# Kernel optimization log

Hardware: AMD Instinct MI355X
Metric: run time of the kernel (lower is better)

Reference implementation:

```python
import jax, jax.numpy as jnp
import numpy as np

K = 8192          # num_codes
D = 256           # code_dim
COMMIT_BETA = 0.25


def setup_inputs() -> dict:
    key = jax.random.key(0)
    k1, k2 = jax.random.split(key)
    z_e = jax.random.normal(k1, (16, 2048, D), dtype=jnp.float32)
    # nn.init.normal_(weight, mean=0, std=1/sqrt(D))
    codebook = jax.random.normal(k2, (K, D), dtype=jnp.float32) * (1.0 / D ** 0.5)
    return {"z_e": z_e, "codebook": codebook}


def reference(z_e, codebook):
    lead_shape = z_e.shape[:-1]
    flat = z_e.reshape(-1, D)                                   # (N, D)
    dist = (
        jnp.sum(flat * flat, axis=-1, keepdims=True)
        - 2.0 * flat @ codebook.T
        + jnp.sum(codebook * codebook, axis=-1)
    )
    idx = jnp.argmin(dist, axis=-1).reshape(lead_shape)          # (...,) int
    z_q = codebook[idx]                                          # (..., D)
    codebook_loss = jnp.mean((z_q - jax.lax.stop_gradient(z_e)) ** 2)
    commit_loss = jnp.mean((z_e - jax.lax.stop_gradient(z_q)) ** 2)
    loss = codebook_loss + COMMIT_BETA * commit_loss
    # straight-through estimator
    z_q_ste = z_e + jax.lax.stop_gradient(z_q - z_e)
    return z_q_ste, idx, loss
```

## Files before the change

kernel.cpp:

```cpp
#include <hip/hip_runtime.h>


#define N_TOK   32768
#define KC      8192
#define DD      256
#define D4      64
#define CSPL    2
#define MT      128
#define EPS1    0.025f
#define EPS2    1e-3f
#define FLAG_CAP 8192
#define CAP2     4096
#define ASTR    40

typedef __bf16    bf16x8 __attribute__((ext_vector_type(8)));
typedef _Float16  f16x8  __attribute__((ext_vector_type(8)));
typedef _Float16  f16x4  __attribute__((ext_vector_type(4)));
typedef float     f32x4  __attribute__((ext_vector_type(4)));

#define GLL(gp, lp) __builtin_amdgcn_global_load_lds(                                   \
    (const __attribute__((address_space(1))) void*)(unsigned long long)(uintptr_t)(gp), \
    (__attribute__((address_space(3))) void*)(unsigned)(uintptr_t)(lp), 16, 0, 0)

#define PK(a, b, HO, LO) do {                                   \
    unsigned ua = __float_as_uint(a), ub = __float_as_uint(b);  \
    unsigned ham = ua & 0xFFFF0000u, hbm = ub & 0xFFFF0000u;    \
    float la = (a) - __uint_as_float(ham);                      \
    float lb = (b) - __uint_as_float(hbm);                      \
    HO = (ua >> 16) | hbm;                                      \
    LO = (__float_as_uint(la) >> 16) | (__float_as_uint(lb) & 0xFFFF0000u); \
} while (0)

__global__ __launch_bounds__(256)
void k_cnorm(const float* __restrict__ cb, float* __restrict__ cnorm,
             double* __restrict__ accum, int* __restrict__ flagc,
             int* __restrict__ flagc2, _Float16* __restrict__ cbf16) {
    if (blockIdx.x == 0 && threadIdx.x == 0) { *accum = 0.0; *flagc = 0; *flagc2 = 0; }
    const int gid  = blockIdx.x * 256 + threadIdx.x;
    const int code = gid >> 6;
    const int lane = threadIdx.x & 63;
    if (code < KC) {
        float4 v = ((const float4*)cb)[code * D4 + lane];
        if (cbf16) {
            f16x4 h;
            h[0] = (_Float16)v.x; h[1] = (_Float16)v.y;
            h[2] = (_Float16)v.z; h[3] = (_Float16)v.w;
            *(f16x4*)(cbf16 + (size_t)code * DD + lane * 4) = h;
        }
        float s = v.x*v.x + v.y*v.y + v.z*v.z + v.w*v.w;
        #pragma unroll
        for (int off = 32; off > 0; off >>= 1) s += __shfl_down(s, off);
        if (lane == 0) cnorm[code] = s;
    }
}

__global__ __launch_bounds__(256)
void k_convert_ze(const float* __restrict__ src, _Float16* __restrict__ dst, int n8) {
    int t = blockIdx.x * 256 + threadIdx.x;
    if (t >= n8) return;
    const float4* s = (const float4*)src;
    float4 v0 = s[2 * t], v1 = s[2 * t + 1];
    f16x8 h;
    h[0] = (_Float16)v0.x; h[1] = (_Float16)v0.y; h[2] = (_Float16)v0.z; h[3] = (_Float16)v0.w;
    h[4] = (_Float16)v1.x; h[5] = (_Float16)v1.y; h[6] = (_Float16)v1.z; h[7] = (_Float16)v1.w;
    ((f16x8*)dst)[t] = h;
}

__global__ __launch_bounds__(256)
void k_argmin_f16(const _Float16* __restrict__ zef, const _Float16* __restrict__ cbf,
                  const float* __restrict__ cnorm, float4* __restrict__ partial) {
    __shared__ __align__(16) char smem[65536];

    const int tid  = threadIdx.x;
    const int lane = tid & 63;
    const int wid  = tid >> 6;
    const int cl   = lane & 15;
    const int kq   = lane >> 4;
    const int m0   = blockIdx.x * MT;
    const int split = blockIdx.y;
    const int c0b  = split * (KC / CSPL);
    const int wrow0 = wid * 32;

    {
        const int lr = lane >> 5;
        const int lc = lane & 31;
        #pragma unroll
        for (int j = 0; j < 16; ++j) {
            int I = wid * 16 + j;
            int r = 2 * I + lr;
            int c = lc ^ (r & 31);
            GLL((const char*)zef + (size_t)(m0 + r) * 512 + c * 16, smem + I * 1024);
        }
    }
    __syncthreads();
    f16x8 afr[2][8];
    #pragma unroll
    for (int mt = 0; mt < 2; ++mt)
        #pragma unroll
        for (int ks = 0; ks < 8; ++ks) {
            int row = wrow0 + mt * 16 + cl;
            int c   = ks * 4 + kq;
            afr[mt][ks] = *(const f16x8*)(smem + row * 512 + (((c ^ (row & 31))) << 4));
        }
    __syncthreads();

    char* bbuf0 = smem;
    char* bbuf1 = smem + 32768;
    const int lr = lane >> 5;
    const int lc = lane & 31;

    #pragma unroll
    for (int j = 0; j < 8; ++j) {
        int I = wid * 8 + j;
        int r = 2 * I + lr;
        int c = lc ^ (r & 31);
        GLL((const char*)cbf + (size_t)(c0b + r) * 512 + c * 16, bbuf0 + I * 1024);
    }
    __syncthreads();

    float best[8], sec[8]; int bidx[8];
    #pragma unroll
    for (int s = 0; s < 8; ++s) { best[s] = 3.4e38f; sec[s] = 3.4e38f; bidx[s] = 0; }

    for (int ch = 0; ch < 64; ++ch) {
        char* cur = (ch & 1) ? bbuf1 : bbuf0;
        char* nxt = (ch & 1) ? bbuf0 : bbuf1;
        if (ch < 63) {
            const int cr0 = c0b + (ch + 1) * 64;
            #pragma unroll
            for (int j = 0; j < 8; ++j) {
                int I = wid * 8 + j;
                int r = 2 * I + lr;
                int c = lc ^ (r & 31);
                GLL((const char*)cbf + (size_t)(cr0 + r) * 512 + c * 16, nxt + I * 1024);
            }
        }

        f32x4 acc[2][4];
        #pragma unroll
        for (int mt = 0; mt < 2; ++mt)
            #pragma unroll
            for (int nt = 0; nt < 4; ++nt)
                acc[mt][nt] = (f32x4){0.f, 0.f, 0.f, 0.f};

        #pragma unroll
        for (int ks = 0; ks < 8; ++ks) {
            f16x8 bfr[4];
            #pragma unroll
            for (int nt = 0; nt < 4; ++nt) {
                int row = nt * 16 + cl;
                int c   = ks * 4 + kq;
                bfr[nt] = *(const f16x8*)(cur + row * 512 + ((c ^ (row & 31)) << 4));
            }
            #pragma unroll
            for (int mt = 0; mt < 2; ++mt)
                #pragma unroll
                for (int nt = 0; nt < 4; ++nt)
                    acc[mt][nt] = __builtin_amdgcn_mfma_f32_16x16x32_f16(afr[mt][ks], bfr[nt], acc[mt][nt], 0, 0, 0);
        }

        const int cc0 = c0b + ch * 64;
        #pragma unroll
        for (int nt = 0; nt < 4; ++nt) {
            const int code = cc0 + nt * 16 + cl;
            const float cn = cnorm[code];
            #pragma unroll
            for (int mt = 0; mt < 2; ++mt)
                #pragma unroll
                for (int r = 0; r < 4; ++r) {
                    float dist = fmaf(-2.f, acc[mt][nt][r], cn);
                    int s = mt * 4 + r;
                    bool lt = dist < best[s];
                    sec[s] = lt ? best[s] : fminf(sec[s], dist);
                    if (lt) { best[s] = dist; bidx[s] = code; }
                }
        }
        __syncthreads();
    }

    #pragma unroll
    for (int m = 1; m < 16; m <<= 1) {
        #pragma unroll
        for (int s = 0; s < 8; ++s) {
            float ob = __shfl_xor(best[s], m);
            int   oi = __shfl_xor(bidx[s], m);
            float os = __shfl_xor(sec[s], m);
            if (ob < best[s] || (ob == best[s] && oi < bidx[s])) {
                sec[s]  = fminf(best[s], os);
                best[s] = ob; bidx[s] = oi;
            } else {
                sec[s]  = fminf(sec[s], ob);
            }
        }
    }
    if (cl == 0) {
        #pragma unroll
        for (int mt = 0; mt < 2; ++mt)
            #pragma unroll
            for (int r = 0; r < 4; ++r) {
                int row = wrow0 + mt * 16 + kq * 4 + r;
                int s = mt * 4 + r;
                partial[(size_t)split * N_TOK + m0 + row] =
                    make_float4(best[s], __int_as_float(bidx[s]), sec[s], 0.f);
            }
    }
}

__global__ __launch_bounds__(256)
void k_combine(const float4* __restrict__ partial, int* __restrict__ idxi,
               float* __restrict__ idxf, int* __restrict__ flagc,
               int* __restrict__ flag_list, int splits, float eps, int cap) {
    const int t = blockIdx.x * 256 + threadIdx.x;
    float B = 3.4e38f, S = 3.4e38f; int I = 0;
    for (int s = 0; s < splits; ++s) {
        float4 p = partial[(size_t)s * N_TOK + t];
        int oi = __float_as_int(p.y);
        if (p.x < B || (p.x == B && oi < I)) { S = fminf(B, p.z); B = p.x; I = oi; }
        else                                  { S = fminf(S, p.x); }
    }
    idxi[t] = I;
    idxf[t] = (float)I;
    if (S - B < eps) {
        int pos = atomicAdd(flagc, 1);
        if (pos < cap) flag_list[pos] = t;
    }
}

__device__ __forceinline__ void stage8(const float* __restrict__ gp,
                                       ushort* __restrict__ h, ushort* __restrict__ l) {
    float4 v0 = *(const float4*)gp;
    float4 v1 = *(const float4*)(gp + 4);
    uint4 hp, lp;
    PK(v0.x, v0.y, hp.x, lp.x);
    PK(v0.z, v0.w, hp.y, lp.y);
    PK(v1.x, v1.y, hp.z, lp.z);
    PK(v1.z, v1.w, hp.w, lp.w);
    *(uint4*)h = hp;
    *(uint4*)l = lp;
}

__global__ __launch_bounds__(256, 2)
void k_argmin2(const float* __restrict__ ze, const float* __restrict__ cb,
               const float* __restrict__ cnorm, const int* __restrict__ flag_list,
               const int* __restrict__ flagc, float4* __restrict__ partial2) {
    int nf = flagc[0]; if (nf > FLAG_CAP) nf = FLAG_CAP;
    const int m0 = blockIdx.x * 64;
    if (m0 >= nf) return;

    __shared__ ushort smem2[(64 + 64 + 256 + 256) * ASTR];
    ushort* Ah = smem2;
    ushort* Al = Ah + 64 * ASTR;
    ushort* Bh = Al + 64 * ASTR;
    ushort* Bl = Bh + 256 * ASTR;

    const int tid  = threadIdx.x;
    const int lane = tid & 63;
    const int wid  = tid >> 6;
    const int cl   = lane & 15;
    const int kq   = lane >> 4;
    const int wn   = wid * 64;
    const int split = blockIdx.y;

    const int r0 = tid >> 2;
    const int g0 = (tid & 3) * 8;
    int tokr = m0 + r0; if (tokr > nf - 1) tokr = nf - 1;
    const int tok = flag_list[tokr];
    const float* zeA = ze + (size_t)tok * DD + g0;

    const int boff = (wn + cl) * ASTR + kq * 8;

    float best[16], sec[16]; int bidx[16];
    #pragma unroll
    for (int s = 0; s < 16; ++s) { best[s] = 3.4e38f; sec[s] = 3.4e38f; bidx[s] = 0; }

    for (int ch = 0; ch < 2; ++ch) {
        const int c0 = split * 512 + ch * 256;
        const float* cbB = cb + (size_t)(c0 + r0) * DD + g0;
        f32x4 acc[4][4];
        #pragma unroll
        for (int mt = 0; mt < 4; ++mt)
            #pragma unroll
            for (int nt = 0; nt < 4; ++nt)
                acc[mt][nt] = (f32x4){0.f, 0.f, 0.f, 0.f};

        for (int ks = 0; ks < 8; ++ks) {
            __syncthreads();
            stage8(zeA + ks * 32, Ah + r0 * ASTR + g0, Al + r0 * ASTR + g0);
            #pragma unroll
            for (int rep = 0; rep < 4; ++rep)
                stage8(cbB + (size_t)rep * 64 * DD + ks * 32,
                       Bh + (r0 + rep * 64) * ASTR + g0, Bl + (r0 + rep * 64) * ASTR + g0);
            __syncthreads();

            bf16x8 bh[4], bl[4];
            #pragma unroll
            for (int nt = 0; nt < 4; ++nt) {
                bh[nt] = *(const bf16x8*)(Bh + boff + nt * 16 * ASTR);
                bl[nt] = *(const bf16x8*)(Bl + boff + nt * 16 * ASTR);
            }
            #pragma unroll
            for (int mt = 0; mt < 4; ++mt) {
                const int ao = (mt * 16 + cl) * ASTR + kq * 8;
                bf16x8 ah = *(const bf16x8*)(Ah + ao);
                bf16x8 al = *(const bf16x8*)(Al + ao);
                #pragma unroll
                for (int nt = 0; nt < 4; ++nt) {
                    acc[mt][nt] = __builtin_amdgcn_mfma_f32_16x16x32_bf16(ah, bh[nt], acc[mt][nt], 0, 0, 0);
                    acc[mt][nt] = __builtin_amdgcn_mfma_f32_16x16x32_bf16(ah, bl[nt], acc[mt][nt], 0, 0, 0);
                    acc[mt][nt] = __builtin_amdgcn_mfma_f32_16x16x32_bf16(al, bh[nt], acc[mt][nt], 0, 0, 0);
                }
            }
        }
        #pragma unroll
        for (int nt = 0; nt < 4; ++nt) {
            const int code = c0 + wn + nt * 16 + cl;
            const float cn = cnorm[code];
            #pragma unroll
            for (int mt = 0; mt < 4; ++mt)
                #pragma unroll
                for (int r = 0; r < 4; ++r) {
                    float dist = fmaf(-2.f, acc[mt][nt][r], cn);
                    int s = mt * 4 + r;
                    bool lt = dist < best[s];
                    sec[s] = lt ? best[s] : fminf(sec[s], dist);
                    if (lt) { best[s] = dist; bidx[s] = code; }
                }
        }
    }

    #pragma unroll
    for (int m = 1; m < 16; m <<= 1) {
        #pragma unroll
        for (int s = 0; s < 16; ++s) {
            float ob = __shfl_xor(best[s], m);
            int   oi = __shfl_xor(bidx[s], m);
            float os = __shfl_xor(sec[s], m);
            if (ob < best[s] || (ob == best[s] && oi < bidx[s])) {
                sec[s]  = fminf(best[s], os);
                best[s] = ob; bidx[s] = oi;
            } else {
                sec[s]  = fminf(sec[s], ob);
            }
        }
    }
    __syncthreads();
    float* mg = (float*)smem2;
    if (cl == 0) {
        #pragma unroll
        for (int mt = 0; mt < 4; ++mt)
            #pragma unroll
            for (int r = 0; r < 4; ++r) {
                int row = mt * 16 + kq * 4 + r;
                int o = (wid * 64 + row) * 4;
                mg[o + 0] = best[mt * 4 + r];
                mg[o + 1] = __int_as_float(bidx[mt * 4 + r]);
                mg[o + 2] = sec[mt * 4 + r];
            }
    }
    __syncthreads();
    if (tid < 64 && m0 + tid < nf) {
        float B = 3.4e38f, S = 3.4e38f; int I = 0;
        #pragma unroll
        for (int j = 0; j < 4; ++j) {
            float b = mg[(j * 64 + tid) * 4];
            int   i = __float_as_int(mg[(j * 64 + tid) * 4 + 1]);
            float s = mg[(j * 64 + tid) * 4 + 2];
            if (b < B || (b == B && i < I)) { S = fminf(B, s); B = b; I = i; }
            else                             { S = fminf(S, b); }
        }
        partial2[(size_t)split * FLAG_CAP + m0 + tid] = make_float4(B, __int_as_float(I), S, 0.f);
    }
}

__global__ __launch_bounds__(256)
void k_combine2(const float4* __restrict__ partial2, const int* __restrict__ flag_list,
                const int* __restrict__ flagc, int* __restrict__ idxi,
                float* __restrict__ idxf, int* __restrict__ flagc2,
                int* __restrict__ list2) {
    int nf = flagc[0]; if (nf > FLAG_CAP) nf = FLAG_CAP;
    const int f = blockIdx.x * 256 + threadIdx.x;
    if (f >= nf) return;
    float B = 3.4e38f, S = 3.4e38f; int I = 0;
    #pragma unroll
    for (int s = 0; s < 16; ++s) {
        float4 p = partial2[(size_t)s * FLAG_CAP + f];
        int oi = __float_as_int(p.y);
        if (p.x < B || (p.x == B && oi < I)) { S = fminf(B, p.z); B = p.x; I = oi; }
        else                                  { S = fminf(S, p.x); }
    }
    const int t = flag_list[f];
    idxi[t] = I;
    idxf[t] = (float)I;
    if (S - B < EPS2) {
        int pos = atomicAdd(flagc2, 1);
        if (pos < CAP2) list2[pos] = t;
    }
}

__global__ __launch_bounds__(256)
void k_rescore_part(const float* __restrict__ ze, const float* __restrict__ cb,
                    const float* __restrict__ cnorm, const int* __restrict__ flagc,
                    const int* __restrict__ flag_list, float2* __restrict__ part3,
                    int cap) {
    __shared__ float xsh[DD];
    __shared__ float2 red[256];
    const int tid = threadIdx.x;
    const int cs  = blockIdx.y;
    int nf = flagc[0]; if (nf > cap) nf = cap;
    for (int f = blockIdx.x; f < nf; f += gridDim.x) {
        const int t = flag_list[f];
        if (tid < 64) *(float4*)&xsh[tid * 4] = ((const float4*)ze)[(size_t)t * D4 + tid];
        __syncthreads();
        const int c = cs * 256 + tid;
        const float4* cr = (const float4*)(cb + (size_t)c * DD);
        float dot = 0.f;
        #pragma unroll 8
        for (int j = 0; j < D4; ++j) {
            float4 cv = cr[j];
            float4 xv = *(const float4*)&xsh[j * 4];
            dot = fmaf(cv.x, xv.x, dot);
            dot = fmaf(cv.y, xv.y, dot);
            dot = fmaf(cv.z, xv.z, dot);
            dot = fmaf(cv.w, xv.w, dot);
        }
        red[tid] = make_float2(fmaf(-2.f, dot, cnorm[c]), __int_as_float(c));
        __syncthreads();
        for (int s = 128; s > 0; s >>= 1) {
            if (tid < s) {
                float2 o = red[tid + s], me = red[tid];
                int oi = __float_as_int(o.y), mi = __float_as_int(me.y);
                if (o.x < me.x || (o.x == me.x && oi < mi)) red[tid] = o;
            }
            __syncthreads();
        }
        if (tid == 0) part3[(size_t)f * 32 + cs] = red[0];
        __syncthreads();
    }
}

__global__ __launch_bounds__(256)
void k_rescore_fin(const float2* __restrict__ part3, const int* __restrict__ flagc,
                   const int* __restrict__ flag_list, int* __restrict__ idxi,
                   float* __restrict__ idxf, int cap) {
    int nf = flagc[0]; if (nf > cap) nf = cap;
    const int f = blockIdx.x * 256 + threadIdx.x;
    if (f >= nf) return;
    float B = 3.4e38f; int I = 0;
    #pragma unroll
    for (int s = 0; s < 32; ++s) {
        float2 p = part3[(size_t)f * 32 + s];
        int oi = __float_as_int(p.y);
        if (p.x < B || (p.x == B && oi < I)) { B = p.x; I = oi; }
    }
    const int t = flag_list[f];
    idxi[t] = I;
    idxf[t] = (float)I;
}

__global__ __launch_bounds__(256)
void k_rescore(const float* __restrict__ ze, const float* __restrict__ cb,
               const float* __restrict__ cnorm, const int* __restrict__ flagc,
               const int* __restrict__ flag_list, int* __restrict__ idxi,
               float* __restrict__ idxf, int cap) {
    __shared__ float xsh[DD];
    __shared__ float2 red[256];
    const int tid = threadIdx.x;
    int nf = flagc[0]; if (nf > cap) nf = cap;
    for (int f = blockIdx.x; f < nf; f += gridDim.x) {
        const int t = flag_list[f];
        if (tid < 64) *(float4*)&xsh[tid * 4] = ((const float4*)ze)[(size_t)t * D4 + tid];
        __syncthreads();
        float B = 3.4e38f; int I = 0;
        for (int c = tid; c < KC; c += 256) {
            const float4* cr = (const float4*)(cb + (size_t)c * DD);
            float dot = 0.f;
            #pragma unroll 8
            for (int j = 0; j < D4; ++j) {
                float4 cv = cr[j];
                float4 xv = *(const float4*)&xsh[j * 4];
                dot = fmaf(cv.x, xv.x, dot);
                dot = fmaf(cv.y, xv.y, dot);
                dot = fmaf(cv.z, xv.z, dot);
                dot = fmaf(cv.w, xv.w, dot);
            }
            float dist = fmaf(-2.f, dot, cnorm[c]);
            if (dist < B) { B = dist; I = c; }
        }
        red[tid] = make_float2(B, __int_as_float(I));
        __syncthreads();
        for (int s = 128; s > 0; s >>= 1) {
            if (tid < s) {
                float2 o = red[tid + s], me = red[tid];
                int oi = __float_as_int(o.y), mi = __float_as_int(me.y);
                if (o.x < me.x || (o.x == me.x && oi < mi)) red[tid] = o;
            }
            __syncthreads();
        }
        if (tid == 0) { int I2 = __float_as_int(red[0].y); idxi[t] = I2; idxf[t] = (float)I2; }
        __syncthreads();
    }
}

__global__ __launch_bounds__(256)
void k_gather(const float* __restrict__ ze, const float* __restrict__ cb,
              const int* __restrict__ idxi, float* __restrict__ zq,
              double* __restrict__ accum) {
    const int tid = threadIdx.x;
    const int t0  = blockIdx.x * 16;
    double dsum = 0.0;
    #pragma unroll
    for (int i = 0; i < 4; ++i) {
        int f = tid + i * 256;
        int row = f >> 6, e = f & 63;
        int t = t0 + row;
        int code = idxi[t];
        float4 zev = ((const float4*)ze)[(size_t)t * D4 + e];
        float4 cbv = ((const float4*)cb)[(size_t)code * D4 + e];
        float dx = cbv.x - zev.x, dy = cbv.y - zev.y;
        float dz = cbv.z - zev.z, dw = cbv.w - zev.w;
        float4 o;
        o.x = zev.x + dx; o.y = zev.y + dy; o.z = zev.z + dz; o.w = zev.w + dw;
        ((float4*)zq)[(size_t)t * D4 + e] = o;
        dsum += (double)dx * dx + (double)dy * dy + (double)dz * dz + (double)dw * dw;
    }
    #pragma unroll
    for (int off = 32; off > 0; off >>= 1) dsum += __shfl_down(dsum, off);
    __shared__ double wsum[4];
    if ((tid & 63) == 0) wsum[tid >> 6] = dsum;
    __syncthreads();
    if (tid == 0) atomicAdd(accum, wsum[0] + wsum[1] + wsum[2] + wsum[3]);
}

__global__ void k_final(const double* __restrict__ accum, float* __restrict__ loss) {
    loss[0] = (float)(accum[0] * (1.25 / 8388608.0));
}

__global__ __launch_bounds__(256, 2)
void k_argmin_fb(const float* __restrict__ ze, const float* __restrict__ cb,
                 const float* __restrict__ cnorm, float4* __restrict__ partial) {
    __shared__ ushort smem[4 * 128 * ASTR];
    ushort* Ah = smem;
    ushort* Al = smem + 128 * ASTR;
    ushort* Bh = smem + 2 * 128 * ASTR;
    ushort* Bl = smem + 3 * 128 * ASTR;

    const int tid  = threadIdx.x;
    const int lane = tid & 63;
    const int wid  = tid >> 6;
    const int cl   = lane & 15;
    const int kq   = lane >> 4;
    const int wm   = (wid & 1) * 64;
    const int wn   = (wid >> 1) * 64;
    const int m0   = blockIdx.x * MT;
    const int split = blockIdx.y;

    const int r0 = tid >> 2;
    const int g0 = (tid & 3) * 8;
    const float* zeA = ze + (size_t)(m0 + r0) * DD + g0;
    const int aoff = (wm + cl) * ASTR + kq * 8;
    const int boff = (wn + cl) * ASTR + kq * 8;

    float best[16], sec[16]; int bidx[16];
    #pragma unroll
    for (int s = 0; s < 16; ++s) { best[s] = 3.4e38f; sec[s] = 3.4e38f; bidx[s] = 0; }

    for (int ch = 0; ch < 4; ++ch) {
        const int c0 = split * 512 + ch * 128;
        const float* cbB = cb + (size_t)(c0 + r0) * DD + g0;
        f32x4 acc[4][4];
        #pragma unroll
        for (int mt = 0; mt < 4; ++mt)
            #pragma unroll
            for (int nt = 0; nt < 4; ++nt)
                acc[mt][nt] = (f32x4){0.f, 0.f, 0.f, 0.f};

        for (int ks = 0; ks < 8; ++ks) {
            __syncthreads();
            stage8(zeA + ks * 32,            Ah + r0 * ASTR + g0, Al + r0 * ASTR + g0);
            stage8(zeA + 64 * DD + ks * 32,  Ah + (r0 + 64) * ASTR + g0, Al + (r0 + 64) * ASTR + g0);
            stage8(cbB + ks * 32,            Bh + r0 * ASTR + g0, Bl + r0 * ASTR + g0);
            stage8(cbB + 64 * DD + ks * 32,  Bh + (r0 + 64) * ASTR + g0, Bl + (r0 + 64) * ASTR + g0);
            __syncthreads();

            bf16x8 bh[4], bl[4];
            #pragma unroll
            for (int nt = 0; nt < 4; ++nt) {
                bh[nt] = *(const bf16x8*)(Bh + boff + nt * 16 * ASTR);
                bl[nt] = *(const bf16x8*)(Bl + boff + nt * 16 * ASTR);
            }
            #pragma unroll
            for (int mt = 0; mt < 4; ++mt) {
                bf16x8 ah = *(const bf16x8*)(Ah + aoff + mt * 16 * ASTR);
                bf16x8 al = *(const bf16x8*)(Al + aoff + mt * 16 * ASTR);
                #pragma unroll
                for (int nt = 0; nt < 4; ++nt) {
                    acc[mt][nt] = __builtin_amdgcn_mfma_f32_16x16x32_bf16(ah, bh[nt], acc[mt][nt], 0, 0, 0);
                    acc[mt][nt] = __builtin_amdgcn_mfma_f32_16x16x32_bf16(ah, bl[nt], acc[mt][nt], 0, 0, 0);
                    acc[mt][nt] = __builtin_amdgcn_mfma_f32_16x16x32_bf16(al, bh[nt], acc[mt][nt], 0, 0, 0);
                }
            }
        }
        #pragma unroll
        for (int nt = 0; nt < 4; ++nt) {
            const int code = c0 + wn + nt * 16 + cl;
            const float cn = cnorm[code];
            #pragma unroll
            for (int mt = 0; mt < 4; ++mt)
                #pragma unroll
                for (int r = 0; r < 4; ++r) {
                    float dist = fmaf(-2.f, acc[mt][nt][r], cn);
                    int s = mt * 4 + r;
                    bool lt = dist < best[s];
                    sec[s] = lt ? best[s] : fminf(sec[s], dist);
                    if (lt) { best[s] = dist; bidx[s] = code; }
                }
        }
    }

    #pragma unroll
    for (int m = 1; m < 16; m <<= 1) {
        #pragma unroll
        for (int s = 0; s < 16; ++s) {
            float ob = __shfl_xor(best[s], m);
            int   oi = __shfl_xor(bidx[s], m);
            float os = __shfl_xor(sec[s], m);
            if (ob < best[s] || (ob == best[s] && oi < bidx[s])) {
                sec[s]  = fminf(best[s], os);
                best[s] = ob; bidx[s] = oi;
            } else {
                sec[s]  = fminf(sec[s], ob);
            }
        }
    }
    __syncthreads();
    float* mg = (float*)smem;
    if (cl == 0) {
        #pragma unroll
        for (int mt = 0; mt < 4; ++mt)
            #pragma unroll
            for (int r = 0; r < 4; ++r) {
                int row = wm + mt * 16 + kq * 4 + r;
                int o = ((wn >> 6) * 128 + row) * 4;
                mg[o + 0] = best[mt * 4 + r];
                mg[o + 1] = __int_as_float(bidx[mt * 4 + r]);
                mg[o + 2] = sec[mt * 4 + r];
            }
    }
    __syncthreads();
    if (tid < MT) {
        float b0 = mg[tid * 4],         s0v = mg[tid * 4 + 2];
        int   i0 = __float_as_int(mg[tid * 4 + 1]);
        float b1 = mg[(128 + tid) * 4], s1v = mg[(128 + tid) * 4 + 2];
        int   i1 = __float_as_int(mg[(128 + tid) * 4 + 1]);
        float B, S; int I;
        if (b1 < b0 || (b1 == b0 && i1 < i0)) { B = b1; I = i1; S = fminf(s1v, b0); }
        else                                   { B = b0; I = i0; S = fminf(s0v, b1); }
        partial[(size_t)split * N_TOK + m0 + tid] = make_float4(B, __int_as_float(I), S, 0.f);
    }
}

extern "C" void kernel_launch(void* const* d_in, const int* in_sizes, int n_in,
                              void* d_out, int out_size, void* d_ws, size_t ws_size,
                              hipStream_t stream) {
    const float* ze = (const float*)d_in[0];
    const float* cb = (const float*)d_in[1];

    float* out      = (float*)d_out;
    float* out_zq   = out;
    float* out_idx  = out + (size_t)N_TOK * DD;
    float* out_loss = out_idx + N_TOK;

    char*   ws    = (char*)d_ws;
    float*  cnorm = (float*)ws;
    int*    idxi  = (int*)(ws + 32768);
    double* accum = (double*)(ws + 163840);
    int*    flagc = (int*)(ws + 163848);
    int*    flagc2= (int*)(ws + 163852);
    int*    flag_list = (int*)(ws + 163856);
    int*    list2     = (int*)(ws + 196624);

    const size_t OFF_ZEF  = 213008;
    const size_t OFF_CBF  = OFF_ZEF + (size_t)N_TOK * DD * 2;
    const size_t OFF_P1   = OFF_CBF + (size_t)KC * DD * 2;
    const size_t OFF_P2   = OFF_P1 + (size_t)CSPL * N_TOK * 16;
    const size_t OFF_P3   = OFF_P2 + 16ull * FLAG_CAP * 16;
    const size_t NEED     = OFF_P3 + (size_t)CAP2 * 32 * 8;

    if (ws_size >= NEED) {
        _Float16* zef = (_Float16*)(ws + OFF_ZEF);
        _Float16* cbf = (_Float16*)(ws + OFF_CBF);
        float4* partial  = (float4*)(ws + OFF_P1);
        float4* partial2 = (float4*)(ws + OFF_P2);
        float2* part3    = (float2*)(ws + OFF_P3);

        hipLaunchKernelGGL(k_cnorm, dim3(KC / 4), dim3(256), 0, stream,
                           cb, cnorm, accum, flagc, flagc2, cbf);
        hipLaunchKernelGGL(k_convert_ze, dim3(N_TOK * DD / 8 / 256), dim3(256), 0, stream,
                           ze, zef, N_TOK * DD / 8);
        hipLaunchKernelGGL(k_argmin_f16, dim3(N_TOK / MT, CSPL), dim3(256), 0, stream,
                           zef, cbf, cnorm, partial);
        hipLaunchKernelGGL(k_combine, dim3(N_TOK / 256), dim3(256), 0, stream,
                           partial, idxi, out_idx, flagc, flag_list, CSPL, EPS1, FLAG_CAP);
        hipLaunchKernelGGL(k_argmin2, dim3(FLAG_CAP / 64, 16), dim3(256), 0, stream,
                           ze, cb, cnorm, flag_list, flagc, partial2);
        hipLaunchKernelGGL(k_combine2, dim3(FLAG_CAP / 256), dim3(256), 0, stream,
                           partial2, flag_list, flagc, idxi, out_idx, flagc2, list2);
        hipLaunchKernelGGL(k_rescore_part, dim3(64, 32), dim3(256), 0, stream,
                           ze, cb, cnorm, flagc2, list2, part3, CAP2);
        hipLaunchKernelGGL(k_rescore_fin, dim3(CAP2 / 256), dim3(256), 0, stream,
                           part3, flagc2, list2, idxi, out_idx, CAP2);
    } else {
        hipLaunchKernelGGL(k_cnorm, dim3(KC / 4), dim3(256), 0, stream,
                           cb, cnorm, accum, flagc, flagc2, (_Float16*)0);
        float4* partial = (float4*)d_out;
        int* fl = (int*)(ws + 163856);
        hipLaunchKernelGGL(k_argmin_fb, dim3(N_TOK / MT, 16), dim3(256), 0, stream,
                           ze, cb, cnorm, partial);
        hipLaunchKernelGGL(k_combine, dim3(N_TOK / 256), dim3(256), 0, stream,
                           partial, idxi, out_idx, flagc, fl, 16, EPS2, FLAG_CAP);
        hipLaunchKernelGGL(k_rescore, dim3(128), dim3(256), 0, stream,
                           ze, cb, cnorm, flagc, fl, idxi, out_idx, FLAG_CAP);
    }

    hipLaunchKernelGGL(k_gather, dim3(N_TOK / 16), dim3(256), 0, stream, ze, cb, idxi, out_zq, accum);
    hipLaunchKernelGGL(k_final,  dim3(1), dim3(1), 0, stream, accum, out_loss);
}
```

Baseline: 417.8 us.

## Shrink f16 argmin code tile for occupancy and precompute bf16 hi/lo codebook

```diff
diff --git a/kernel.cpp b/kernel.cpp
--- a/kernel.cpp
+++ b/kernel.cpp
@@ -5,7 +5,7 @@
 #define KC      8192
 #define DD      256
 #define D4      64
-#define CSPL    2
+#define CSPL    4
 #define MT      128
 #define EPS1    0.025f
 #define EPS2    1e-3f
@@ -34,7 +34,8 @@
 __global__ __launch_bounds__(256)
 void k_cnorm(const float* __restrict__ cb, float* __restrict__ cnorm,
              double* __restrict__ accum, int* __restrict__ flagc,
-             int* __restrict__ flagc2, _Float16* __restrict__ cbf16) {
+             int* __restrict__ flagc2, _Float16* __restrict__ cbf16,
+             ushort* __restrict__ cbh, ushort* __restrict__ cbl) {
     if (blockIdx.x == 0 && threadIdx.x == 0) { *accum = 0.0; *flagc = 0; *flagc2 = 0; }
     const int gid  = blockIdx.x * 256 + threadIdx.x;
     const int code = gid >> 6;
@@ -47,6 +48,15 @@
             h[2] = (_Float16)v.z; h[3] = (_Float16)v.w;
             *(f16x4*)(cbf16 + (size_t)code * DD + lane * 4) = h;
         }
+        if (cbh) {
+            unsigned h01, l01, h23, l23;
+            PK(v.x, v.y, h01, l01);
+            PK(v.z, v.w, h23, l23);
+            uint2 hp; hp.x = h01; hp.y = h23;
+            uint2 lp; lp.x = l01; lp.y = l23;
+            *(uint2*)(cbh + (size_t)code * DD + lane * 4) = hp;
+            *(uint2*)(cbl + (size_t)code * DD + lane * 4) = lp;
+        }
         float s = v.x*v.x + v.y*v.y + v.z*v.z + v.w*v.w;
         #pragma unroll
         for (int off = 32; off > 0; off >>= 1) s += __shfl_down(s, off);
@@ -66,10 +76,10 @@
     ((f16x8*)dst)[t] = h;
 }
 
-__global__ __launch_bounds__(256)
+__global__ __launch_bounds__(256, 4)
 void k_argmin_f16(const _Float16* __restrict__ zef, const _Float16* __restrict__ cbf,
                   const float* __restrict__ cnorm, float4* __restrict__ partial) {
-    __shared__ __align__(16) char smem[65536];
+    __shared__ __align__(16) char smem[32768];
 
     const int tid  = threadIdx.x;
     const int lane = tid & 63;
@@ -80,42 +90,47 @@
     const int split = blockIdx.y;
     const int c0b  = split * (KC / CSPL);
     const int wrow0 = wid * 32;
-
-    {
-        const int lr = lane >> 5;
-        const int lc = lane & 31;
-        #pragma unroll
-        for (int j = 0; j < 16; ++j) {
-            int I = wid * 16 + j;
+    const int lr   = lane >> 5;
+    const int lc   = lane & 31;
+
+    f16x8 afr[2][8];
+    #pragma unroll
+    for (int h = 0; h < 2; ++h) {
+        #pragma unroll
+        for (int j = 0; j < 8; ++j) {
+            int I = wid * 8 + j;
             int r = 2 * I + lr;
             int c = lc ^ (r & 31);
-            GLL((const char*)zef + (size_t)(m0 + r) * 512 + c * 16, smem + I * 1024);
-        }
-    }
-    __syncthreads();
-    f16x8 afr[2][8];
-    #pragma unroll
-    for (int mt = 0; mt < 2; ++mt)
-        #pragma unroll
-        for (int ks = 0; ks < 8; ++ks) {
-            int row = wrow0 + mt * 16 + cl;
-            int c   = ks * 4 + kq;
-            afr[mt][ks] = *(const f16x8*)(smem + row * 512 + (((c ^ (row & 31))) << 4));
-        }
-    __syncthreads();
+            GLL((const char*)zef + (size_t)(m0 + h * 64 + r) * 512 + c * 16,
+                smem + I * 1024);
+        }
+        __syncthreads();
+        if ((wid >> 1) == h) {
+            #pragma unroll
+            for (int mt = 0; mt < 2; ++mt)
+                #pragma unroll
+                for (int ks = 0; ks < 8; ++ks) {
+                    int rr = (wid & 1) * 32 + mt * 16 + cl;
+                    int c  = ks * 4 + kq;
+                    afr[mt][ks] = *(const f16x8*)(smem + rr * 512 + ((c ^ (rr & 31)) << 4));
+                }
+        }
+        __syncthreads();
+    }
 
     char* bbuf0 = smem;
-    char* bbuf1 = smem + 32768;
-    const int lr = lane >> 5;
-    const int lc = lane & 31;
-
-    #pragma unroll
-    for (int j = 0; j < 8; ++j) {
-        int I = wid * 8 + j;
+    char* bbuf1 = smem + 16384;
+    unsigned boffs[4];
+    #pragma unroll
+    for (int j = 0; j < 4; ++j) {
+        int I = wid * 4 + j;
         int r = 2 * I + lr;
-        int c = lc ^ (r & 31);
-        GLL((const char*)cbf + (size_t)(c0b + r) * 512 + c * 16, bbuf0 + I * 1024);
-    }
+        boffs[j] = (unsigned)r * 512u + (unsigned)((lc ^ (r & 31)) << 4);
+    }
+
+    #pragma unroll
+    for (int j = 0; j < 4; ++j)
+        GLL((const char*)cbf + (size_t)c0b * 512 + boffs[j], bbuf0 + (wid * 4 + j) * 1024);
     __syncthreads();
 
     float best[8], sec[8]; int bidx[8];
@@ -126,28 +141,24 @@
         char* cur = (ch & 1) ? bbuf1 : bbuf0;
         char* nxt = (ch & 1) ? bbuf0 : bbuf1;
         if (ch < 63) {
-            const int cr0 = c0b + (ch + 1) * 64;
-            #pragma unroll
-            for (int j = 0; j < 8; ++j) {
-                int I = wid * 8 + j;
-                int r = 2 * I + lr;
-                int c = lc ^ (r & 31);
-                GLL((const char*)cbf + (size_t)(cr0 + r) * 512 + c * 16, nxt + I * 1024);
-            }
-        }
-
-        f32x4 acc[2][4];
+            const size_t gb = (size_t)(c0b + (ch + 1) * 32) * 512;
+            #pragma unroll
+            for (int j = 0; j < 4; ++j)
+                GLL((const char*)cbf + gb + boffs[j], nxt + (wid * 4 + j) * 1024);
+        }
+
+        f32x4 acc[2][2];
         #pragma unroll
         for (int mt = 0; mt < 2; ++mt)
             #pragma unroll
-            for (int nt = 0; nt < 4; ++nt)
+            for (int nt = 0; nt < 2; ++nt)
                 acc[mt][nt] = (f32x4){0.f, 0.f, 0.f, 0.f};
 
         #pragma unroll
         for (int ks = 0; ks < 8; ++ks) {
-            f16x8 bfr[4];
-            #pragma unroll
-            for (int nt = 0; nt < 4; ++nt) {
+            f16x8 bfr[2];
+            #pragma unroll
+            for (int nt = 0; nt < 2; ++nt) {
                 int row = nt * 16 + cl;
                 int c   = ks * 4 + kq;
                 bfr[nt] = *(const f16x8*)(cur + row * 512 + ((c ^ (row & 31)) << 4));
@@ -155,13 +166,13 @@
             #pragma unroll
             for (int mt = 0; mt < 2; ++mt)
                 #pragma unroll
-                for (int nt = 0; nt < 4; ++nt)
+                for (int nt = 0; nt < 2; ++nt)
                     acc[mt][nt] = __builtin_amdgcn_mfma_f32_16x16x32_f16(afr[mt][ks], bfr[nt], acc[mt][nt], 0, 0, 0);
         }
 
-        const int cc0 = c0b + ch * 64;
-        #pragma unroll
-        for (int nt = 0; nt < 4; ++nt) {
+        const int cc0 = c0b + ch * 32;
+        #pragma unroll
+        for (int nt = 0; nt < 2; ++nt) {
             const int code = cc0 + nt * 16 + cl;
             const float cn = cnorm[code];
             #pragma unroll
@@ -240,9 +251,10 @@
 }
 
 __global__ __launch_bounds__(256, 2)
-void k_argmin2(const float* __restrict__ ze, const float* __restrict__ cb,
-               const float* __restrict__ cnorm, const int* __restrict__ flag_list,
-               const int* __restrict__ flagc, float4* __restrict__ partial2) {
+void k_argmin2(const float* __restrict__ ze, const ushort* __restrict__ cbh,
+               const ushort* __restrict__ cbl, const float* __restrict__ cnorm,
+               const int* __restrict__ flag_list, const int* __restrict__ flagc,
+               float4* __restrict__ partial2) {
     int nf = flagc[0]; if (nf > FLAG_CAP) nf = FLAG_CAP;
     const int m0 = blockIdx.x * 64;
     if (m0 >= nf) return;
@@ -275,7 +287,6 @@
 
     for (int ch = 0; ch < 2; ++ch) {
         const int c0 = split * 512 + ch * 256;
-        const float* cbB = cb + (size_t)(c0 + r0) * DD + g0;
         f32x4 acc[4][4];
         #pragma unroll
         for (int mt = 0; mt < 4; ++mt)
@@ -287,9 +298,11 @@
             __syncthreads();
             stage8(zeA + ks * 32, Ah + r0 * ASTR + g0, Al + r0 * ASTR + g0);
             #pragma unroll
-            for (int rep = 0; rep < 4; ++rep)
-                stage8(cbB + (size_t)rep * 64 * DD + ks * 32,
-                       Bh + (r0 + rep * 64) * ASTR + g0, Bl + (r0 + rep * 64) * ASTR + g0);
+            for (int rep = 0; rep < 4; ++rep) {
+                const size_t crow = (size_t)(c0 + rep * 64 + r0) * DD + ks * 32 + g0;
+                *(uint4*)(Bh + (r0 + rep * 64) * ASTR + g0) = *(const uint4*)(cbh + crow);
+                *(uint4*)(Bl + (r0 + rep * 64) * ASTR + g0) = *(const uint4*)(cbl + crow);
+            }
             __syncthreads();
 
             bf16x8 bh[4], bl[4];
@@ -684,7 +697,9 @@
     const size_t OFF_P1   = OFF_CBF + (size_t)KC * DD * 2;
     const size_t OFF_P2   = OFF_P1 + (size_t)CSPL * N_TOK * 16;
     const size_t OFF_P3   = OFF_P2 + 16ull * FLAG_CAP * 16;
-    const size_t NEED     = OFF_P3 + (size_t)CAP2 * 32 * 8;
+    const size_t OFF_CBH  = OFF_P3 + (size_t)CAP2 * 32 * 8;
+    const size_t OFF_CBL  = OFF_CBH + (size_t)KC * DD * 2;
+    const size_t NEED     = OFF_CBL + (size_t)KC * DD * 2;
 
     if (ws_size >= NEED) {
         _Float16* zef = (_Float16*)(ws + OFF_ZEF);
@@ -692,9 +707,11 @@
         float4* partial  = (float4*)(ws + OFF_P1);
         float4* partial2 = (float4*)(ws + OFF_P2);
         float2* part3    = (float2*)(ws + OFF_P3);
+        ushort* cbh = (ushort*)(ws + OFF_CBH);
+        ushort* cbl = (ushort*)(ws + OFF_CBL);
 
         hipLaunchKernelGGL(k_cnorm, dim3(KC / 4), dim3(256), 0, stream,
-                           cb, cnorm, accum, flagc, flagc2, cbf);
+                           cb, cnorm, accum, flagc, flagc2, cbf, cbh, cbl);
         hipLaunchKernelGGL(k_convert_ze, dim3(N_TOK * DD / 8 / 256), dim3(256), 0, stream,
                            ze, zef, N_TOK * DD / 8);
         hipLaunchKernelGGL(k_argmin_f16, dim3(N_TOK / MT, CSPL), dim3(256), 0, stream,
@@ -702,7 +719,7 @@
         hipLaunchKernelGGL(k_combine, dim3(N_TOK / 256), dim3(256), 0, stream,
                            partial, idxi, out_idx, flagc, flag_list, CSPL, EPS1, FLAG_CAP);
         hipLaunchKernelGGL(k_argmin2, dim3(FLAG_CAP / 64, 16), dim3(256), 0, stream,
-                           ze, cb, cnorm, flag_list, flagc, partial2);
+                           ze, cbh, cbl, cnorm, flag_list, flagc, partial2);
         hipLaunchKernelGGL(k_combine2, dim3(FLAG_CAP / 256), dim3(256), 0, stream,
                            partial2, flag_list, flagc, idxi, out_idx, flagc2, list2);
         hipLaunchKernelGGL(k_rescore_part, dim3(64, 32), dim3(256), 0, stream,
@@ -711,7 +728,7 @@
                            part3, flagc2, list2, idxi, out_idx, CAP2);
     } else {
         hipLaunchKernelGGL(k_cnorm, dim3(KC / 4), dim3(256), 0, stream,
-                           cb, cnorm, accum, flagc, flagc2, (_Float16*)0);
+                           cb, cnorm, accum, flagc, flagc2, (_Float16*)0, (ushort*)0, (ushort*)0);
         float4* partial = (float4*)d_out;
         int* fl = (int*)(ws + 163856);
         hipLaunchKernelGGL(k_argmin_fb, dim3(N_TOK / MT, 16), dim3(256), 0, stream,
```

Result: slower. 450.8 us (+7.9%).
